# Performance work log

Hardware: AMD Instinct MI355X
Metric: run time of the kernel (lower is better)

Reference implementation:

```python
import jax, jax.numpy as jnp
import numpy as np

NUM_NODES_G1 = 60000
NUM_NODES_G2 = 50000
NUM_REL = 16
NUM_BASES = 4
DIM = 128  # node_dim == hidden_dim == final_dim
L_COMMON = 100


def _concept_layer(x, edge_index):
    # Gather-based concept propagation: x_i <- x_i + mean_{j in N(i)} x_j
    src, dst = edge_index[0], edge_index[1]
    n = x.shape[0]
    agg = jax.ops.segment_sum(x[src], dst, num_segments=n)
    deg = jax.ops.segment_sum(jnp.ones((src.shape[0],), x.dtype), dst, num_segments=n)
    return x + agg / jnp.clip(deg, 1.0)[:, None]


def _rgcn_layer(x, edge_index, edge_type, basis, comp, root, bias):
    # Basis-decomposed RGCN: out_i = x_i @ root + bias + sum_r (1/|N_i^r|) sum_{j in N_i^r} x_j @ W_r,
    # W_r = sum_b comp[r,b] * basis[b]. Reorder: scatter comp-weighted x[src] per basis, then one GEMM per basis.
    src, dst = edge_index[0], edge_index[1]
    n = x.shape[0]
    e = src.shape[0]
    seg = dst * NUM_REL + edge_type  # per-(node, relation) bucket
    cnt = jax.ops.segment_sum(jnp.ones((e,), x.dtype), seg, num_segments=n * NUM_REL)
    norm = 1.0 / jnp.clip(cnt, 1.0)
    coef = comp[edge_type] * norm[seg][:, None]  # [E, B]
    xsrc = x[src]  # [E, D] -- dominant gather traffic
    out = x @ root + bias
    for b in range(NUM_BASES):  # small fixed loop over bases
        agg_b = jax.ops.segment_sum(xsrc * coef[:, b:b + 1], dst, num_segments=n)
        out = out + agg_b @ basis[b]
    return out


def setup_inputs() -> dict:
    key = jax.random.key(0)
    ks = jax.random.split(key, 16)
    e2, e1 = 800000, 800000
    return {
        "edge_index_g2": jax.random.randint(ks[0], (2, e2), 0, NUM_NODES_G2),
        "edge_type_g2": jax.random.randint(ks[1], (e2,), 0, NUM_REL),
        "edge_index_g1": jax.random.randint(ks[2], (2, e1), 0, NUM_NODES_G1),
        "left_common": jax.random.randint(ks[3], (L_COMMON,), 0, NUM_NODES_G1),
        "all_node_embedding": jax.random.normal(ks[4], (NUM_NODES_G1, DIM), jnp.float32),
        "basis1": jax.random.normal(ks[5], (NUM_BASES, DIM, DIM), jnp.float32) * 0.05,
        "comp1": jax.random.normal(ks[6], (NUM_REL, NUM_BASES), jnp.float32),
        "root1": jax.random.normal(ks[7], (DIM, DIM), jnp.float32) * 0.05,
        "bias1": jnp.zeros((DIM,), jnp.float32),
        "basis2": jax.random.normal(ks[8], (NUM_BASES, DIM, DIM), jnp.float32) * 0.05,
        "comp2": jax.random.normal(ks[9], (NUM_REL, NUM_BASES), jnp.float32),
        "root2": jax.random.normal(ks[10], (DIM, DIM), jnp.float32) * 0.05,
        "bias2": jnp.zeros((DIM,), jnp.float32),
        "weights": jax.random.uniform(ks[11], (DIM, 1), jnp.float32),
    }


def reference(edge_index_g2, edge_type_g2, edge_index_g1, left_common,
              all_node_embedding, basis1, comp1, root1, bias1,
              basis2, comp2, root2, bias2, weights):
    x_g1 = jax.nn.relu(_concept_layer(all_node_embedding, edge_index_g1))
    x = x_g1[:NUM_NODES_G2]
    x = _rgcn_layer(x, edge_index_g2, edge_type_g2, basis1, comp1, root1, bias1)
    x = jax.nn.relu(x)  # relu_use == 1
    x_g2 = _rgcn_layer(x, edge_index_g2, edge_type_g2, basis2, comp2, root2, bias2)
    ty = x_g1[left_common]  # [L, D]
    # mul_def outer elementwise product followed by matmul with weights collapses to one contraction:
    # logits[n,l] = sum_d x_g2[n,d] * ty[l,d] * w[d]
    logits = jnp.einsum('nd,ld,d->nl', x_g2, ty, weights[:, 0])
    return jax.nn.softmax(logits, axis=1)
```

## Files before the change

kernel.cpp:

```cpp
#include <hip/hip_runtime.h>
#include <hip/hip_bf16.h>
#include <math.h>

#define N1 60000
#define N2 50000
#define DIM 128
#define NREL 16
#define NB 4
#define LCOM 100
#define LPAD 112

typedef __attribute__((ext_vector_type(8))) short short8;
typedef __attribute__((ext_vector_type(4))) float f32x4;

__device__ __forceinline__ float bf2f(unsigned short u) {
    union { unsigned int i; float f; } c; c.i = ((unsigned int)u) << 16; return c.f;
}
__device__ __forceinline__ unsigned short f2bf(float f) {
    union { float f; unsigned int i; } c; c.f = f;
    unsigned int r = c.i + 0x7FFF + ((c.i >> 16) & 1);
    return (unsigned short)(r >> 16);
}
__device__ __forceinline__ void split8(float4 a, float4 b, short8& h, short8& l) {
    float f[8] = {a.x, a.y, a.z, a.w, b.x, b.y, b.z, b.w};
#pragma unroll
    for (int j = 0; j < 8; j++) {
        unsigned short hh = f2bf(f[j]);
        h[j] = (short)hh;
        l[j] = (short)f2bf(f[j] - bf2f(hh));
    }
}

__global__ void k_prep_w(const float* __restrict__ root, const float* __restrict__ basis,
                         unsigned short* __restrict__ Wh, unsigned short* __restrict__ Wl) {
    int t = blockIdx.x * blockDim.x + threadIdx.x;
    if (t >= 640 * 128) return;
    int k = t >> 7, n = t & 127;
    float v = (k < 128) ? root[k * 128 + n] : basis[(k - 128) * 128 + n];
    unsigned short h = f2bf(v);
    Wh[n * 640 + k] = h;
    Wl[n * 640 + k] = f2bf(v - bf2f(h));
}

__global__ void k_hist_deg(const int* __restrict__ ei, int* __restrict__ deg, int E) {
    int e = blockIdx.x * blockDim.x + threadIdx.x;
    if (e >= E) return;
    atomicAdd(deg + ei[E + e], 1);
}

__global__ void k_hist_dt(const int* __restrict__ ei, const int* __restrict__ et,
                          int* __restrict__ cnt, int E) {
    int e = blockIdx.x * blockDim.x + threadIdx.x;
    if (e >= E) return;
    atomicAdd(cnt + ei[E + e] * NREL + et[e], 1);
}

__global__ void k_deg_from_cnt(const int* __restrict__ cnt, int* __restrict__ deg, int n) {
    int i = blockIdx.x * blockDim.x + threadIdx.x;
    if (i >= n) return;
    int s = 0;
#pragma unroll
    for (int t = 0; t < NREL; t++) s += cnt[i * NREL + t];
    deg[i] = s;
}

__global__ __launch_bounds__(256) void k_scan_p1(const int* __restrict__ in,
                                                 int* __restrict__ bsum, int n) {
    __shared__ int red[256];
    int base = blockIdx.x * 1024;
    int tid = threadIdx.x;
    int s = 0;
#pragma unroll
    for (int j = 0; j < 4; j++) {
        int i = base + tid * 4 + j;
        if (i < n) s += in[i];
    }
    red[tid] = s;
    __syncthreads();
    for (int d = 128; d; d >>= 1) {
        if (tid < d) red[tid] += red[tid + d];
        __syncthreads();
    }
    if (tid == 0) bsum[blockIdx.x] = red[0];
}

__global__ __launch_bounds__(64) void k_scan_p2(const int* __restrict__ bsum,
                                                int* __restrict__ boff,
                                                int* __restrict__ off, int nb, int n) {
    __shared__ int s[64];
    int tid = threadIdx.x;
    int v = (tid < nb) ? bsum[tid] : 0;
    s[tid] = v;
    __syncthreads();
    for (int d = 1; d < 64; d <<= 1) {
        int t = (tid >= d) ? s[tid - d] : 0;
        __syncthreads();
        s[tid] += t;
        __syncthreads();
    }
    if (tid < nb) boff[tid] = s[tid] - v;
    if (tid == 63) off[n] = s[63];
}

__global__ __launch_bounds__(256) void k_scan_p3(const int* __restrict__ in,
                                                 const int* __restrict__ boff,
                                                 int* __restrict__ off,
                                                 int* __restrict__ cur, int n) {
    __shared__ int red[256];
    int base = blockIdx.x * 1024;
    int tid = threadIdx.x;
    int v[4];
    int s = 0;
#pragma unroll
    for (int j = 0; j < 4; j++) {
        int i = base + tid * 4 + j;
        v[j] = (i < n) ? in[i] : 0;
        s += v[j];
    }
    red[tid] = s;
    __syncthreads();
    for (int d = 1; d < 256; d <<= 1) {
        int t = (tid >= d) ? red[tid - d] : 0;
        __syncthreads();
        red[tid] += t;
        __syncthreads();
    }
    int run = boff[blockIdx.x] + red[tid] - s;
#pragma unroll
    for (int j = 0; j < 4; j++) {
        int i = base + tid * 4 + j;
        if (i < n) {
            off[i] = run; cur[i] = run;
            run += v[j];
        }
    }
}

__global__ void k_csr_scatter1(const int* __restrict__ ei, int* __restrict__ cur,
                               int* __restrict__ elist, int E) {
    int e = blockIdx.x * blockDim.x + threadIdx.x;
    if (e >= E) return;
    int pos = atomicAdd(cur + ei[E + e], 1);
    elist[pos] = ei[e];
}

__global__ void k_csr_scatter2(const int* __restrict__ ei, const int* __restrict__ et,
                               int* __restrict__ cur, int* __restrict__ elist, int E) {
    int e = blockIdx.x * blockDim.x + threadIdx.x;
    if (e >= E) return;
    int pos = atomicAdd(cur + ei[E + e], 1);
    elist[pos] = (ei[e] << 4) | et[e];
}

__global__ __launch_bounds__(256) void k_concept_gather(const float* __restrict__ emb,
                                                        const int* __restrict__ off,
                                                        const int* __restrict__ elist,
                                                        float* __restrict__ xg1, int n) {
    int node = blockIdx.x * 4 + (threadIdx.x >> 6);
    int lane = threadIdx.x & 63;
    if (node >= n) return;
    int s0 = off[node], s1 = off[node + 1];
    float2 acc = {0.f, 0.f};
    int i = s0;
    for (; i + 1 < s1; i += 2) {
        int sa = elist[i], sb = elist[i + 1];
        float2 va = *(const float2*)(emb + (size_t)sa * DIM + lane * 2);
        float2 vb = *(const float2*)(emb + (size_t)sb * DIM + lane * 2);
        acc.x += va.x + vb.x; acc.y += va.y + vb.y;
    }
    if (i < s1) {
        int sa = elist[i];
        float2 va = *(const float2*)(emb + (size_t)sa * DIM + lane * 2);
        acc.x += va.x; acc.y += va.y;
    }
    float inv = 1.0f / (float)max(s1 - s0, 1);
    float2 e = *(const float2*)(emb + (size_t)node * DIM + lane * 2);
    float2 o = {fmaxf(e.x + acc.x * inv, 0.f), fmaxf(e.y + acc.y * inv, 0.f)};
    *(float2*)(xg1 + (size_t)node * DIM + lane * 2) = o;
}

__global__ __launch_bounds__(64) void k_tyw(const float* __restrict__ emb,
                                            const int* __restrict__ off,
                                            const int* __restrict__ elist,
                                            const int* __restrict__ lc,
                                            const float* __restrict__ w,
                                            unsigned short* __restrict__ tyh,
                                            unsigned short* __restrict__ tyl) {
    int l = blockIdx.x;
    int lane = threadIdx.x;
    int d0 = lane * 2;
    if (l >= LCOM) {
        ushort2 z = {0, 0};
        *(ushort2*)(tyh + (size_t)l * 128 + d0) = z;
        *(ushort2*)(tyl + (size_t)l * 128 + d0) = z;
        return;
    }
    int row = lc[l];
    int s0 = off[row], s1 = off[row + 1];
    float2 acc = {0.f, 0.f};
    for (int i = s0; i < s1; i++) {
        int s = elist[i];
        float2 v = *(const float2*)(emb + (size_t)s * DIM + lane * 2);
        acc.x += v.x; acc.y += v.y;
    }
    float inv = 1.0f / (float)max(s1 - s0, 1);
    float2 e = *(const float2*)(emb + (size_t)row * DIM + lane * 2);
    float v0 = fmaxf(e.x + acc.x * inv, 0.f) * w[d0];
    float v1 = fmaxf(e.y + acc.y * inv, 0.f) * w[d0 + 1];
    unsigned short h0 = f2bf(v0), h1 = f2bf(v1);
    ushort2 hh = {h0, h1};
    ushort2 ll = {f2bf(v0 - bf2f(h0)), f2bf(v1 - bf2f(h1))};
    *(ushort2*)(tyh + (size_t)l * 128 + d0) = hh;
    *(ushort2*)(tyl + (size_t)l * 128 + d0) = ll;
}

__global__ __launch_bounds__(256) void k_rgcn_gather(const float* __restrict__ x,
                                                     const int* __restrict__ off,
                                                     const int* __restrict__ elist,
                                                     const int* __restrict__ cnt,
                                                     const float* __restrict__ comp,
                                                     float* __restrict__ agg, int n) {
    int node = blockIdx.x * 4 + (threadIdx.x >> 6);
    int lane = threadIdx.x & 63;
    if (node >= n) return;
    int s0 = off[node], s1 = off[node + 1];
    const int* cb = cnt + node * NREL;
    float2 a0 = {0, 0}, a1 = {0, 0}, a2 = {0, 0}, a3 = {0, 0};
    int i = s0;
    for (; i + 1 < s1; i += 2) {
        int pa = elist[i], pb = elist[i + 1];
        int sa = pa >> 4, ta = pa & 15;
        int sb = pb >> 4, tb = pb & 15;
        float2 va = *(const float2*)(x + (size_t)sa * DIM + lane * 2);
        float2 vb = *(const float2*)(x + (size_t)sb * DIM + lane * 2);
        float na = 1.0f / fmaxf((float)cb[ta], 1.0f);
        float nb = 1.0f / fmaxf((float)cb[tb], 1.0f);
        float c;
        c = comp[ta * NB + 0] * na; a0.x = fmaf(c, va.x, a0.x); a0.y = fmaf(c, va.y, a0.y);
        c = comp[ta * NB + 1] * na; a1.x = fmaf(c, va.x, a1.x); a1.y = fmaf(c, va.y, a1.y);
        c = comp[ta * NB + 2] * na; a2.x = fmaf(c, va.x, a2.x); a2.y = fmaf(c, va.y, a2.y);
        c = comp[ta * NB + 3] * na; a3.x = fmaf(c, va.x, a3.x); a3.y = fmaf(c, va.y, a3.y);
        c = comp[tb * NB + 0] * nb; a0.x = fmaf(c, vb.x, a0.x); a0.y = fmaf(c, vb.y, a0.y);
        c = comp[tb * NB + 1] * nb; a1.x = fmaf(c, vb.x, a1.x); a1.y = fmaf(c, vb.y, a1.y);
        c = comp[tb * NB + 2] * nb; a2.x = fmaf(c, vb.x, a2.x); a2.y = fmaf(c, vb.y, a2.y);
        c = comp[tb * NB + 3] * nb; a3.x = fmaf(c, vb.x, a3.x); a3.y = fmaf(c, vb.y, a3.y);
    }
    if (i < s1) {
        int pa = elist[i];
        int sa = pa >> 4, ta = pa & 15;
        float2 va = *(const float2*)(x + (size_t)sa * DIM + lane * 2);
        float na = 1.0f / fmaxf((float)cb[ta], 1.0f);
        float c;
        c = comp[ta * NB + 0] * na; a0.x = fmaf(c, va.x, a0.x); a0.y = fmaf(c, va.y, a0.y);
        c = comp[ta * NB + 1] * na; a1.x = fmaf(c, va.x, a1.x); a1.y = fmaf(c, va.y, a1.y);
        c = comp[ta * NB + 2] * na; a2.x = fmaf(c, va.x, a2.x); a2.y = fmaf(c, va.y, a2.y);
        c = comp[ta * NB + 3] * na; a3.x = fmaf(c, va.x, a3.x); a3.y = fmaf(c, va.y, a3.y);
    }
    float* o = agg + (size_t)node * (NB * DIM) + lane * 2;
    *(float2*)(o + 0 * DIM) = a0;
    *(float2*)(o + 1 * DIM) = a1;
    *(float2*)(o + 2 * DIM) = a2;
    *(float2*)(o + 3 * DIM) = a3;
}

#define LDSK 40
__global__ __launch_bounds__(256) void k_gemm(const float* __restrict__ x,
                                              const float* __restrict__ agg,
                                              const unsigned short* __restrict__ Wh,
                                              const unsigned short* __restrict__ Wl,
                                              const float* __restrict__ bias,
                                              float* __restrict__ out, int relu) {
    __shared__ __align__(16) short Ah[128 * LDSK];
    __shared__ __align__(16) short Al[128 * LDSK];
    __shared__ __align__(16) short Bh[128 * LDSK];
    __shared__ __align__(16) short Bl[128 * LDSK];
    int tid = threadIdx.x;
    int lane = tid & 63, wid = tid >> 6;
    int wave_m = wid >> 1, wave_n = wid & 1;
    int l15 = lane & 15, quad = lane >> 4;
    int row0 = blockIdx.x * 128;

    int srow = tid >> 1, skh = (tid & 1) * 16;

    f32x4 acc[4][4] = {};
    for (int k0 = 0; k0 < 640; k0 += 32) {
        {
            int rg = row0 + srow;
            float4 q0 = {0, 0, 0, 0}, q1 = q0, q2 = q0, q3 = q0;
            if (rg < N2) {
                const float* src = (k0 < 128) ? (x + (size_t)rg * 128 + k0 + skh)
                                              : (agg + (size_t)rg * 512 + (k0 - 128) + skh);
                q0 = *(const float4*)(src + 0);
                q1 = *(const float4*)(src + 4);
                q2 = *(const float4*)(src + 8);
                q3 = *(const float4*)(src + 12);
            }
            short8 h0, l0, h1, l1;
            split8(q0, q1, h0, l0);
            split8(q2, q3, h1, l1);
            *(short8*)(&Ah[srow * LDSK + skh]) = h0;
            *(short8*)(&Ah[srow * LDSK + skh + 8]) = h1;
            *(short8*)(&Al[srow * LDSK + skh]) = l0;
            *(short8*)(&Al[srow * LDSK + skh + 8]) = l1;
        }
        {
            const unsigned short* sh = Wh + (size_t)srow * 640 + k0 + skh;
            const unsigned short* sl = Wl + (size_t)srow * 640 + k0 + skh;
            *(short8*)(&Bh[srow * LDSK + skh]) = *(const short8*)(sh);
            *(short8*)(&Bh[srow * LDSK + skh + 8]) = *(const short8*)(sh + 8);
            *(short8*)(&Bl[srow * LDSK + skh]) = *(const short8*)(sl);
            *(short8*)(&Bl[srow * LDSK + skh + 8]) = *(const short8*)(sl + 8);
        }
        __syncthreads();
        short8 ah[4], al[4], bh[4], bl[4];
#pragma unroll
        for (int i = 0; i < 4; i++) {
            int ro = (wave_m * 64 + i * 16 + l15) * LDSK + quad * 8;
            ah[i] = *(const short8*)(&Ah[ro]);
            al[i] = *(const short8*)(&Al[ro]);
        }
#pragma unroll
        for (int j = 0; j < 4; j++) {
            int ro = (wave_n * 64 + j * 16 + l15) * LDSK + quad * 8;
            bh[j] = *(const short8*)(&Bh[ro]);
            bl[j] = *(const short8*)(&Bl[ro]);
        }
#pragma unroll
        for (int i = 0; i < 4; i++)
#pragma unroll
            for (int j = 0; j < 4; j++) {
                acc[i][j] = __builtin_amdgcn_mfma_f32_16x16x32_bf16(al[i], bh[j], acc[i][j], 0, 0, 0);
                acc[i][j] = __builtin_amdgcn_mfma_f32_16x16x32_bf16(ah[i], bl[j], acc[i][j], 0, 0, 0);
                acc[i][j] = __builtin_amdgcn_mfma_f32_16x16x32_bf16(ah[i], bh[j], acc[i][j], 0, 0, 0);
            }
        __syncthreads();
    }
#pragma unroll
    for (int j = 0; j < 4; j++) {
        int gcol = wave_n * 64 + j * 16 + l15;
        float bv = bias[gcol];
#pragma unroll
        for (int i = 0; i < 4; i++) {
            int grow_base = row0 + wave_m * 64 + i * 16 + quad * 4;
#pragma unroll
            for (int r = 0; r < 4; r++) {
                int grow = grow_base + r;
                if (grow >= N2) continue;
                float v = acc[i][j][r] + bv;
                if (relu) v = fmaxf(v, 0.f);
                out[(size_t)grow * 128 + gcol] = v;
            }
        }
    }
}

__global__ __launch_bounds__(256) void k_logits(const float* __restrict__ h2,
                                                const unsigned short* __restrict__ tyh,
                                                const unsigned short* __restrict__ tyl,
                                                float* __restrict__ out, int M) {
    int wid = threadIdx.x >> 6, lane = threadIdx.x & 63;
    int l15 = lane & 15, quad = lane >> 4;
    int row0w = blockIdx.x * 64 + wid * 16;
    int arow = min(row0w + l15, M - 1);
    f32x4 acc[7] = {};
#pragma unroll
    for (int k0 = 0; k0 < 128; k0 += 32) {
        const float* ap = h2 + (size_t)arow * 128 + k0 + quad * 8;
        float4 q0 = *(const float4*)(ap);
        float4 q1 = *(const float4*)(ap + 4);
        short8 ah, al;
        split8(q0, q1, ah, al);
#pragma unroll
        for (int j = 0; j < 7; j++) {
            size_t bo = (size_t)(j * 16 + l15) * 128 + k0 + quad * 8;
            short8 bh = *(const short8*)(tyh + bo);
            short8 bl = *(const short8*)(tyl + bo);
            acc[j] = __builtin_amdgcn_mfma_f32_16x16x32_bf16(al, bh, acc[j], 0, 0, 0);
            acc[j] = __builtin_amdgcn_mfma_f32_16x16x32_bf16(ah, bl, acc[j], 0, 0, 0);
            acc[j] = __builtin_amdgcn_mfma_f32_16x16x32_bf16(ah, bh, acc[j], 0, 0, 0);
        }
    }
    bool v6 = (l15 < LCOM - 96);
#pragma unroll
    for (int r = 0; r < 4; r++) {
        int grow = row0w + quad * 4 + r;
        float m = -INFINITY;
#pragma unroll
        for (int j = 0; j < 6; j++) m = fmaxf(m, acc[j][r]);
        if (v6) m = fmaxf(m, acc[6][r]);
        m = fmaxf(m, __shfl_xor(m, 8, 64));
        m = fmaxf(m, __shfl_xor(m, 4, 64));
        m = fmaxf(m, __shfl_xor(m, 2, 64));
        m = fmaxf(m, __shfl_xor(m, 1, 64));
        float e[7];
        float s = 0.f;
#pragma unroll
        for (int j = 0; j < 6; j++) { e[j] = __expf(acc[j][r] - m); s += e[j]; }
        e[6] = v6 ? __expf(acc[6][r] - m) : 0.f;
        s += e[6];
        s += __shfl_xor(s, 8, 64);
        s += __shfl_xor(s, 4, 64);
        s += __shfl_xor(s, 2, 64);
        s += __shfl_xor(s, 1, 64);
        float inv = 1.0f / s;
        if (grow < M) {
#pragma unroll
            for (int j = 0; j < 6; j++) out[(size_t)grow * LCOM + j * 16 + l15] = e[j] * inv;
            if (v6) out[(size_t)grow * LCOM + 96 + l15] = e[6] * inv;
        }
    }
}

extern "C" void kernel_launch(void* const* d_in, const int* in_sizes, int n_in,
                              void* d_out, int out_size, void* d_ws, size_t ws_size,
                              hipStream_t stream) {
    const int* ei2 = (const int*)d_in[0];
    const int* et2 = (const int*)d_in[1];
    const int* ei1 = (const int*)d_in[2];
    const int* lc = (const int*)d_in[3];
    const float* emb = (const float*)d_in[4];
    const float* basis1 = (const float*)d_in[5];
    const float* comp1 = (const float*)d_in[6];
    const float* root1 = (const float*)d_in[7];
    const float* bias1 = (const float*)d_in[8];
    const float* basis2 = (const float*)d_in[9];
    const float* comp2 = (const float*)d_in[10];
    const float* root2 = (const float*)d_in[11];
    const float* bias2 = (const float*)d_in[12];
    const float* wts = (const float*)d_in[13];
    float* out = (float*)d_out;
    int E2 = in_sizes[0] / 2, E1 = in_sizes[2] / 2;

    float* ws = (float*)d_ws;
    float* xg1 = ws;
    float* h1 = xg1 + 6400000;
    float* agg = h1 + 6400000;
    unsigned short* tyh = (unsigned short*)(agg + 25600000);
    unsigned short* tyl = tyh + LPAD * 128;
    unsigned short* Wh1 = tyl + LPAD * 128;
    unsigned short* Wl1 = Wh1 + 81920;
    unsigned short* Wh2 = Wl1 + 81920;
    unsigned short* Wl2 = Wh2 + 81920;
    int* ipool = (int*)(Wl2 + 81920);
    int* deg1 = ipool;
    int* off1 = deg1 + 60000;
    int* cur1 = off1 + 60001;
    int* elist1 = cur1 + 60000;
    int* cnt2 = elist1 + 800000;
    int* deg2 = cnt2 + 800000;
    int* off2 = deg2 + 50000;
    int* cur2 = off2 + 50001;
    int* elist2 = cur2 + 50000;
    int* bsum1 = elist2 + 800000;
    int* boff1 = bsum1 + 64;
    int* bsum2 = boff1 + 64;
    int* boff2 = bsum2 + 64;
    float* h2 = xg1;

    const int NB1 = (N1 + 1023) / 1024;
    const int NB2 = (N2 + 1023) / 1024;

    k_prep_w<<<(640 * 128 + 255) / 256, 256, 0, stream>>>(root1, basis1, Wh1, Wl1);
    k_prep_w<<<(640 * 128 + 255) / 256, 256, 0, stream>>>(root2, basis2, Wh2, Wl2);

    hipMemsetAsync(deg1, 0, 60000 * sizeof(int), stream);
    k_hist_deg<<<(E1 + 255) / 256, 256, 0, stream>>>(ei1, deg1, E1);
    k_scan_p1<<<NB1, 256, 0, stream>>>(deg1, bsum1, N1);
    k_scan_p2<<<1, 64, 0, stream>>>(bsum1, boff1, off1, NB1, N1);
    k_scan_p3<<<NB1, 256, 0, stream>>>(deg1, boff1, off1, cur1, N1);
    k_csr_scatter1<<<(E1 + 255) / 256, 256, 0, stream>>>(ei1, cur1, elist1, E1);
    k_concept_gather<<<(N2 + 3) / 4, 256, 0, stream>>>(emb, off1, elist1, xg1, N2);
    k_tyw<<<LPAD, 64, 0, stream>>>(emb, off1, elist1, lc, wts, tyh, tyl);

    hipMemsetAsync(cnt2, 0, 800000 * sizeof(int), stream);
    k_hist_dt<<<(E2 + 255) / 256, 256, 0, stream>>>(ei2, et2, cnt2, E2);
    k_deg_from_cnt<<<(N2 + 255) / 256, 256, 0, stream>>>(cnt2, deg2, N2);
    k_scan_p1<<<NB2, 256, 0, stream>>>(deg2, bsum2, N2);
    k_scan_p2<<<1, 64, 0, stream>>>(bsum2, boff2, off2, NB2, N2);
    k_scan_p3<<<NB2, 256, 0, stream>>>(deg2, boff2, off2, cur2, N2);
    k_csr_scatter2<<<(E2 + 255) / 256, 256, 0, stream>>>(ei2, et2, cur2, elist2, E2);

    k_rgcn_gather<<<(N2 + 3) / 4, 256, 0, stream>>>(xg1, off2, elist2, cnt2, comp1, agg, N2);
    k_gemm<<<(N2 + 127) / 128, 256, 0, stream>>>(xg1, agg, Wh1, Wl1, bias1, h1, 1);

    k_rgcn_gather<<<(N2 + 3) / 4, 256, 0, stream>>>(h1, off2, elist2, cnt2, comp2, agg, N2);
    k_gemm<<<(N2 + 127) / 128, 256, 0, stream>>>(h1, agg, Wh2, Wl2, bias2, h2, 0);

    k_logits<<<(N2 + 63) / 64, 256, 0, stream>>>(h2, tyh, tyl, out, N2);
}
```

Before: 653.6 us.

## Widen gathers to float4 with half-wave edge split and precomputed per-edge norms

```diff
diff --git a/kernel.cpp b/kernel.cpp
--- a/kernel.cpp
+++ b/kernel.cpp
@@ -145,11 +145,14 @@
 }
 
 __global__ void k_csr_scatter2(const int* __restrict__ ei, const int* __restrict__ et,
-                               int* __restrict__ cur, int* __restrict__ elist, int E) {
+                               const int* __restrict__ cnt, int* __restrict__ cur,
+                               int* __restrict__ elist, float* __restrict__ nrmv, int E) {
     int e = blockIdx.x * blockDim.x + threadIdx.x;
     if (e >= E) return;
-    int pos = atomicAdd(cur + ei[E + e], 1);
-    elist[pos] = (ei[e] << 4) | et[e];
+    int dst = ei[E + e], t = et[e];
+    int pos = atomicAdd(cur + dst, 1);
+    elist[pos] = (ei[e] << 4) | t;
+    nrmv[pos] = 1.0f / fmaxf((float)cnt[dst * NREL + t], 1.0f);
 }
 
 __global__ __launch_bounds__(256) void k_concept_gather(const float* __restrict__ emb,
@@ -159,24 +162,36 @@
     int node = blockIdx.x * 4 + (threadIdx.x >> 6);
     int lane = threadIdx.x & 63;
     if (node >= n) return;
+    int half = lane >> 5, d4 = (lane & 31) * 4;
     int s0 = off[node], s1 = off[node + 1];
-    float2 acc = {0.f, 0.f};
+    float4 acc = {0.f, 0.f, 0.f, 0.f};
     int i = s0;
-    for (; i + 1 < s1; i += 2) {
-        int sa = elist[i], sb = elist[i + 1];
-        float2 va = *(const float2*)(emb + (size_t)sa * DIM + lane * 2);
-        float2 vb = *(const float2*)(emb + (size_t)sb * DIM + lane * 2);
+    for (; i + 4 <= s1; i += 4) {
+        int sa = elist[i + half];
+        int sb = elist[i + 2 + half];
+        float4 va = *(const float4*)(emb + (size_t)sa * DIM + d4);
+        float4 vb = *(const float4*)(emb + (size_t)sb * DIM + d4);
         acc.x += va.x + vb.x; acc.y += va.y + vb.y;
-    }
-    if (i < s1) {
-        int sa = elist[i];
-        float2 va = *(const float2*)(emb + (size_t)sa * DIM + lane * 2);
-        acc.x += va.x; acc.y += va.y;
-    }
-    float inv = 1.0f / (float)max(s1 - s0, 1);
-    float2 e = *(const float2*)(emb + (size_t)node * DIM + lane * 2);
-    float2 o = {fmaxf(e.x + acc.x * inv, 0.f), fmaxf(e.y + acc.y * inv, 0.f)};
-    *(float2*)(xg1 + (size_t)node * DIM + lane * 2) = o;
+        acc.z += va.z + vb.z; acc.w += va.w + vb.w;
+    }
+    for (; i < s1; i += 2) {
+        int e = i + half;
+        bool ok = e < s1;
+        int s = elist[ok ? e : i];
+        float4 v = *(const float4*)(emb + (size_t)s * DIM + d4);
+        if (ok) { acc.x += v.x; acc.y += v.y; acc.z += v.z; acc.w += v.w; }
+    }
+    acc.x += __shfl_xor(acc.x, 32, 64);
+    acc.y += __shfl_xor(acc.y, 32, 64);
+    acc.z += __shfl_xor(acc.z, 32, 64);
+    acc.w += __shfl_xor(acc.w, 32, 64);
+    if (half == 0) {
+        float inv = 1.0f / (float)max(s1 - s0, 1);
+        float4 e = *(const float4*)(emb + (size_t)node * DIM + d4);
+        float4 o = {fmaxf(e.x + acc.x * inv, 0.f), fmaxf(e.y + acc.y * inv, 0.f),
+                    fmaxf(e.z + acc.z * inv, 0.f), fmaxf(e.w + acc.w * inv, 0.f)};
+        *(float4*)(xg1 + (size_t)node * DIM + d4) = o;
+    }
 }
 
 __global__ __launch_bounds__(64) void k_tyw(const float* __restrict__ emb,
@@ -217,50 +232,62 @@
 __global__ __launch_bounds__(256) void k_rgcn_gather(const float* __restrict__ x,
                                                      const int* __restrict__ off,
                                                      const int* __restrict__ elist,
-                                                     const int* __restrict__ cnt,
+                                                     const float* __restrict__ nrmv,
                                                      const float* __restrict__ comp,
                                                      float* __restrict__ agg, int n) {
+    __shared__ float scomp[NREL * NB];
+    if (threadIdx.x < NREL * NB) scomp[threadIdx.x] = comp[threadIdx.x];
+    __syncthreads();
     int node = blockIdx.x * 4 + (threadIdx.x >> 6);
     int lane = threadIdx.x & 63;
     if (node >= n) return;
+    int half = lane >> 5, d4 = (lane & 31) * 4;
     int s0 = off[node], s1 = off[node + 1];
-    const int* cb = cnt + node * NREL;
-    float2 a0 = {0, 0}, a1 = {0, 0}, a2 = {0, 0}, a3 = {0, 0};
+    float4 a0 = {0, 0, 0, 0}, a1 = a0, a2 = a0, a3 = a0;
     int i = s0;
-    for (; i + 1 < s1; i += 2) {
-        int pa = elist[i], pb = elist[i + 1];
-        int sa = pa >> 4, ta = pa & 15;
-        int sb = pb >> 4, tb = pb & 15;
-        float2 va = *(const float2*)(x + (size_t)sa * DIM + lane * 2);
-        float2 vb = *(const float2*)(x + (size_t)sb * DIM + lane * 2);
-        float na = 1.0f / fmaxf((float)cb[ta], 1.0f);
-        float nb = 1.0f / fmaxf((float)cb[tb], 1.0f);
-        float c;
-        c = comp[ta * NB + 0] * na; a0.x = fmaf(c, va.x, a0.x); a0.y = fmaf(c, va.y, a0.y);
-        c = comp[ta * NB + 1] * na; a1.x = fmaf(c, va.x, a1.x); a1.y = fmaf(c, va.y, a1.y);
-        c = comp[ta * NB + 2] * na; a2.x = fmaf(c, va.x, a2.x); a2.y = fmaf(c, va.y, a2.y);
-        c = comp[ta * NB + 3] * na; a3.x = fmaf(c, va.x, a3.x); a3.y = fmaf(c, va.y, a3.y);
-        c = comp[tb * NB + 0] * nb; a0.x = fmaf(c, vb.x, a0.x); a0.y = fmaf(c, vb.y, a0.y);
-        c = comp[tb * NB + 1] * nb; a1.x = fmaf(c, vb.x, a1.x); a1.y = fmaf(c, vb.y, a1.y);
-        c = comp[tb * NB + 2] * nb; a2.x = fmaf(c, vb.x, a2.x); a2.y = fmaf(c, vb.y, a2.y);
-        c = comp[tb * NB + 3] * nb; a3.x = fmaf(c, vb.x, a3.x); a3.y = fmaf(c, vb.y, a3.y);
-    }
-    if (i < s1) {
-        int pa = elist[i];
-        int sa = pa >> 4, ta = pa & 15;
-        float2 va = *(const float2*)(x + (size_t)sa * DIM + lane * 2);
-        float na = 1.0f / fmaxf((float)cb[ta], 1.0f);
-        float c;
-        c = comp[ta * NB + 0] * na; a0.x = fmaf(c, va.x, a0.x); a0.y = fmaf(c, va.y, a0.y);
-        c = comp[ta * NB + 1] * na; a1.x = fmaf(c, va.x, a1.x); a1.y = fmaf(c, va.y, a1.y);
-        c = comp[ta * NB + 2] * na; a2.x = fmaf(c, va.x, a2.x); a2.y = fmaf(c, va.y, a2.y);
-        c = comp[ta * NB + 3] * na; a3.x = fmaf(c, va.x, a3.x); a3.y = fmaf(c, va.y, a3.y);
-    }
-    float* o = agg + (size_t)node * (NB * DIM) + lane * 2;
-    *(float2*)(o + 0 * DIM) = a0;
-    *(float2*)(o + 1 * DIM) = a1;
-    *(float2*)(o + 2 * DIM) = a2;
-    *(float2*)(o + 3 * DIM) = a3;
+#define RG_EDGE(E_IDX, NRM)                                                    \
+    {                                                                          \
+        int p = elist[E_IDX];                                                  \
+        float nr = (NRM);                                                      \
+        int s = p >> 4, t = p & 15;                                            \
+        float4 cf = *(const float4*)(scomp + t * 4);                           \
+        float4 v = *(const float4*)(x + (size_t)s * DIM + d4);                 \
+        float c0 = cf.x * nr, c1 = cf.y * nr, c2 = cf.z * nr, c3 = cf.w * nr;  \
+        a0.x = fmaf(c0, v.x, a0.x); a0.y = fmaf(c0, v.y, a0.y);                \
+        a0.z = fmaf(c0, v.z, a0.z); a0.w = fmaf(c0, v.w, a0.w);                \
+        a1.x = fmaf(c1, v.x, a1.x); a1.y = fmaf(c1, v.y, a1.y);                \
+        a1.z = fmaf(c1, v.z, a1.z); a1.w = fmaf(c1, v.w, a1.w);                \
+        a2.x = fmaf(c2, v.x, a2.x); a2.y = fmaf(c2, v.y, a2.y);                \
+        a2.z = fmaf(c2, v.z, a2.z); a2.w = fmaf(c2, v.w, a2.w);                \
+        a3.x = fmaf(c3, v.x, a3.x); a3.y = fmaf(c3, v.y, a3.y);                \
+        a3.z = fmaf(c3, v.z, a3.z); a3.w = fmaf(c3, v.w, a3.w);                \
+    }
+    for (; i + 4 <= s1; i += 4) {
+        RG_EDGE(i + half, nrmv[i + half]);
+        RG_EDGE(i + 2 + half, nrmv[i + 2 + half]);
+    }
+    for (; i < s1; i += 2) {
+        int e = i + half;
+        bool ok = e < s1;
+        int ei_ = ok ? e : i;
+        RG_EDGE(ei_, ok ? nrmv[ei_] : 0.0f);
+    }
+#undef RG_EDGE
+    a0.x += __shfl_xor(a0.x, 32, 64); a0.y += __shfl_xor(a0.y, 32, 64);
+    a0.z += __shfl_xor(a0.z, 32, 64); a0.w += __shfl_xor(a0.w, 32, 64);
+    a1.x += __shfl_xor(a1.x, 32, 64); a1.y += __shfl_xor(a1.y, 32, 64);
+    a1.z += __shfl_xor(a1.z, 32, 64); a1.w += __shfl_xor(a1.w, 32, 64);
+    a2.x += __shfl_xor(a2.x, 32, 64); a2.y += __shfl_xor(a2.y, 32, 64);
+    a2.z += __shfl_xor(a2.z, 32, 64); a2.w += __shfl_xor(a2.w, 32, 64);
+    a3.x += __shfl_xor(a3.x, 32, 64); a3.y += __shfl_xor(a3.y, 32, 64);
+    a3.z += __shfl_xor(a3.z, 32, 64); a3.w += __shfl_xor(a3.w, 32, 64);
+    if (half == 0) {
+        float* o = agg + (size_t)node * (NB * DIM) + d4;
+        *(float4*)(o + 0 * DIM) = a0;
+        *(float4*)(o + 1 * DIM) = a1;
+        *(float4*)(o + 2 * DIM) = a2;
+        *(float4*)(o + 3 * DIM) = a3;
+    }
 }
 
 #define LDSK 40
@@ -435,7 +462,8 @@
     float* xg1 = ws;
     float* h1 = xg1 + 6400000;
     float* agg = h1 + 6400000;
-    unsigned short* tyh = (unsigned short*)(agg + 25600000);
+    float* nrmv = agg + 25600000;
+    unsigned short* tyh = (unsigned short*)(nrmv + 800000);
     unsigned short* tyl = tyh + LPAD * 128;
     unsigned short* Wh1 = tyl + LPAD * 128;
     unsigned short* Wl1 = Wh1 + 81920;
@@ -478,12 +506,12 @@
     k_scan_p1<<<NB2, 256, 0, stream>>>(deg2, bsum2, N2);
     k_scan_p2<<<1, 64, 0, stream>>>(bsum2, boff2, off2, NB2, N2);
     k_scan_p3<<<NB2, 256, 0, stream>>>(deg2, boff2, off2, cur2, N2);
-    k_csr_scatter2<<<(E2 + 255) / 256, 256, 0, stream>>>(ei2, et2, cur2, elist2, E2);
-
-    k_rgcn_gather<<<(N2 + 3) / 4, 256, 0, stream>>>(xg1, off2, elist2, cnt2, comp1, agg, N2);
+    k_csr_scatter2<<<(E2 + 255) / 256, 256, 0, stream>>>(ei2, et2, cnt2, cur2, elist2, nrmv, E2);
+
+    k_rgcn_gather<<<(N2 + 3) / 4, 256, 0, stream>>>(xg1, off2, elist2, nrmv, comp1, agg, N2);
     k_gemm<<<(N2 + 127) / 128, 256, 0, stream>>>(xg1, agg, Wh1, Wl1, bias1, h1, 1);
 
-    k_rgcn_gather<<<(N2 + 3) / 4, 256, 0, stream>>>(h1, off2, elist2, cnt2, comp2, agg, N2);
+    k_rgcn_gather<<<(N2 + 3) / 4, 256, 0, stream>>>(h1, off2, elist2, nrmv, comp2, agg, N2);
     k_gemm<<<(N2 + 127) / 128, 256, 0, stream>>>(h1, agg, Wh2, Wl2, bias2, h2, 0);
 
     k_logits<<<(N2 + 63) / 64, 256, 0, stream>>>(h2, tyh, tyl, out, N2);
```

Result: faster. 629.2 us (-3.7%).
